# Kernel tuning notes

Measured on AMD Instinct MI355X. Metric: run time of the kernel, lower is better.

The kernel has to match this reference:

```python
import jax, jax.numpy as jnp
import numpy as np

N, C, T, V = 16, 64, 512, 25
R, O, S = 8, 64, 3  # rel_channels, out_channels, num_subset


def setup_inputs() -> dict:
    key = jax.random.key(0)
    ks = jax.random.split(key, 12)
    sc = 0.05
    return {
        "x": jax.random.normal(ks[0], (N, C, T, V), jnp.float32),
        "A": jax.random.normal(ks[1], (S, V, V), jnp.float32) * 0.1,
        "alpha": jax.random.normal(ks[2], (1,), jnp.float32) * 0.1,
        "w1": jax.random.normal(ks[3], (S, R, C), jnp.float32) * sc,
        "b1": jax.random.normal(ks[4], (S, R), jnp.float32) * sc,
        "w2": jax.random.normal(ks[5], (S, R, C), jnp.float32) * sc,
        "b2": jax.random.normal(ks[6], (S, R), jnp.float32) * sc,
        "w3": jax.random.normal(ks[7], (S, O, C), jnp.float32) * sc,
        "b3": jax.random.normal(ks[8], (S, O), jnp.float32) * sc,
        "w4": jax.random.normal(ks[9], (S, O, R), jnp.float32) * sc,
        "b4": jax.random.normal(ks[10], (S, O), jnp.float32) * sc,
        "sparse": 0,
    }


def _mask(w, thr):
    # SparseConv2d: magnitude-threshold the 1x1 conv weights at runtime.
    return jnp.where(jnp.abs(w) > thr, w, jnp.zeros_like(w))


def reference(x, A, alpha, w1, b1, w2, b2, w3, b3, w4, b4, sparse):
    thr = jnp.float32(sparse)

    def conv1x1(w, b, inp):  # w [o,c], b [o], inp [n,c,t,v] -> [n,o,t,v]
        return jnp.einsum('oc,nctv->notv', _mask(w, thr), inp) + b[None, :, None, None]

    y = None
    for i in range(A.shape[0]):
        x1 = conv1x1(w1[i], b1[i], x).mean(-2)          # [n,r,v]
        x2 = conv1x1(w2[i], b2[i], x).mean(-2)          # [n,r,v]
        x3 = conv1x1(w3[i], b3[i], x)                   # [n,o,t,v]
        att = jnp.tanh(x1[..., :, None] - x2[..., None, :])  # [n,r,v,v]
        a = jnp.einsum('or,nruv->nouv', _mask(w4[i], thr), att) + b4[i][None, :, None, None]
        a = a * alpha + A[i][None, None]                # [n,o,v,v]
        z = jnp.einsum('ncuv,nctu->nctv', a, x3)        # node aggregation
        y = z if y is None else y + z
    # in_channels == out_channels -> residual is identity
    return jax.nn.relu(y + x)
```

## Files before the change

kernel.cpp:

```cpp
#include <hip/hip_runtime.h>
#include <cmath>

typedef __bf16 bf16x8 __attribute__((ext_vector_type(8)));
typedef float f32x4 __attribute__((ext_vector_type(4)));

namespace {
constexpr int kN = 16, kC = 64, kT = 512, kV = 25, kS = 3, kR = 8, kO = 64;
constexpr int kTV = kT * kV;
constexpr int kTT = 16;
constexpr size_t WS_AFRAG = 102400;
constexpr size_t WS_W3F = WS_AFRAG + (size_t)48 * 131072;
}

__device__ __forceinline__ int swzA(int col, int cbyte) {
  return ((col << 7) + cbyte) ^ ((col & 7) << 4);
}
__device__ __forceinline__ int swzB(int c, int t, int ubyte) {
  return 65536 + (c << 10) + (((t << 6) + ubyte) ^ ((t & 7) << 4));
}

__global__ __launch_bounds__(512) void k1_mean(const float* __restrict__ x,
                                               float* __restrict__ xm) {
  const int bid = blockIdx.x;
  __shared__ float tile[kTV];
  __shared__ float part[25][20];
  const int tid = threadIdx.x;
  const float4* xg4 = (const float4*)(x + (size_t)bid * kTV);
  for (int i4 = tid; i4 < 3200; i4 += 512) ((float4*)tile)[i4] = xg4[i4];
  __syncthreads();
  if (tid < 500) {
    const int v = tid / 20, k = tid % 20;
    float psum = 0.f;
    for (int t = k; t < kT; t += 20) psum += tile[t * 25 + v];
    part[v][k] = psum;
  }
  __syncthreads();
  if (tid < 25) {
    float s = 0.f;
#pragma unroll
    for (int kk = 0; kk < 20; ++kk) s += part[tid][kk];
    xm[bid * 25 + tid] = s * (1.f / 512.f);
  }
}

__global__ __launch_bounds__(256) void k2_attn(
    const float* __restrict__ xm, const float* __restrict__ Ag,
    const float* __restrict__ alpha, const float* __restrict__ w1,
    const float* __restrict__ b1, const float* __restrict__ w2,
    const float* __restrict__ b2, const float* __restrict__ w3,
    const float* __restrict__ w4, const float* __restrict__ b4,
    const int* __restrict__ sparse, unsigned char* __restrict__ ws) {
  const float thr = (float)sparse[0];
  const int b = blockIdx.x;
  const int s = b >> 6, n = (b >> 2) & 15, q = b & 3;
  __shared__ float xm_l[1600];
  __shared__ float x1_l[200], x2_l[200];
  __shared__ float att_l[8 * 625];
  __shared__ float attsum_l[200];
  __shared__ float ag_l[625];
  __shared__ float acs_l[25];
  __shared__ float w4_l[512];
  const int tid = threadIdx.x;
  for (int i = tid; i < 1600; i += 256) xm_l[i] = xm[n * 1600 + i];
  for (int i = tid; i < 512; i += 256) {
    float w = w4[s * 512 + i];
    w4_l[i] = (fabsf(w) > thr) ? w : 0.f;
  }
  for (int i = tid; i < 625; i += 256) ag_l[i] = Ag[s * 625 + i];
  __syncthreads();
  for (int i = tid; i < 400; i += 256) {
    int which = i / 200, idx = i % 200, r = idx / 25, u = idx % 25;
    const float* wrow = (which == 0 ? w1 : w2) + (s * 8 + r) * 64;
    float acc = 0.f;
    for (int cc = 0; cc < 64; ++cc) {
      float w = wrow[cc];
      w = (fabsf(w) > thr) ? w : 0.f;
      acc += w * xm_l[cc * 25 + u];
    }
    acc += (which == 0 ? b1 : b2)[s * 8 + r];
    if (which == 0) x1_l[idx] = acc;
    else x2_l[idx] = acc;
  }
  __syncthreads();
  for (int i = tid; i < 8 * 625; i += 256) {
    int r = i / 625, uv = i % 625, u = uv / 25, v = uv % 25;
    att_l[i] = tanhf(x1_l[r * 25 + u] - x2_l[r * 25 + v]);
  }
  __syncthreads();
  if (tid < 200) {
    int r = tid / 25, v = tid % 25;
    float sum = 0.f;
    for (int u = 0; u < 25; ++u) sum += att_l[r * 625 + u * 25 + v];
    attsum_l[tid] = sum;
  } else if (tid < 225) {
    int v = tid - 200;
    float sum = 0.f;
    for (int u = 0; u < 25; ++u) sum += ag_l[u * 25 + v];
    acs_l[v] = sum;
  }
  __syncthreads();
  const float al = alpha[0];
  unsigned char* afrag = ws + WS_AFRAG + (size_t)(s * 16 + n) * 131072;
  for (int slot = q * 2048 + tid; slot < (q + 1) * 2048; slot += 256) {
    int c = slot >> 7, vt = (slot >> 6) & 1, l = slot & 63;
    int v = vt * 16 + (l & 15), g = l >> 4;
    bf16x8 out;
    if (v < 25) {
      float b4v = b4[s * 64 + c];
#pragma unroll
      for (int j = 0; j < 8; ++j) {
        int u = g * 8 + j;
        float val = 0.f;
        if (u < 25) {
          float acc = 0.f;
#pragma unroll
          for (int r = 0; r < 8; ++r) acc += w4_l[c * 8 + r] * att_l[r * 625 + u * 25 + v];
          val = al * (acc + b4v) + ag_l[u * 25 + v];
        } else if (u == 25) {
          float acc = 0.f;
#pragma unroll
          for (int r = 0; r < 8; ++r) acc += w4_l[c * 8 + r] * attsum_l[r * 25 + v];
          val = al * acc + 25.f * al * b4v + acs_l[v];
        }
        out[j] = (__bf16)val;
      }
    } else {
#pragma unroll
      for (int j = 0; j < 8; ++j) out[j] = (__bf16)0.f;
    }
    *(bf16x8*)(afrag + (size_t)slot * 16) = out;
  }
  if (n == 0 && tid < 128) {
    unsigned char* w3f = ws + WS_W3F + (size_t)s * 8192;
    int slot = q * 128 + tid;
    int ot = slot >> 7, ks = (slot >> 6) & 1, l = slot & 63;
    int o = ot * 16 + (l & 15), g = l >> 4;
    bf16x8 out;
#pragma unroll
    for (int j = 0; j < 8; ++j) {
      int cp = ks * 32 + g * 8 + j;
      float w = w3[(s * 64 + o) * 64 + cp];
      out[j] = (__bf16)((fabsf(w) > thr) ? w : 0.f);
    }
    *(bf16x8*)(w3f + slot * 16) = out;
  }
}

__global__ __launch_bounds__(512, 2) void k3_main(const float* __restrict__ x,
                                                  const float* __restrict__ b3,
                                                  const unsigned char* __restrict__ ws,
                                                  float* __restrict__ y) {
  const int n = blockIdx.x;
  const int tb = blockIdx.y;
  extern __shared__ __align__(16) unsigned char smem[];
  const int tid = threadIdx.x;
  const int w = tid >> 6, l = tid & 63, g = l >> 4, l15 = l & 15;

  const float4* xg4 = (const float4*)(x + (size_t)n * kC * kTV);

  for (int idx = tid; idx < 3072; idx += 512) {
    int c = idx / 48, r = idx % 48, t = r / 3, ub = 52 + (r % 3) * 4;
    *(unsigned int*)(smem + swzB(c, t, ub)) = 0u;
  }
  for (int i4 = tid; i4 < 6400; i4 += 512) {
    int c = i4 / 100, r4 = i4 % 100;
    float4 vv = xg4[c * 3200 + tb * 100 + r4];
    float vals[4] = {vv.x, vv.y, vv.z, vv.w};
    int lin = r4 * 4;
#pragma unroll
    for (int kk = 0; kk < 4; ++kk) {
      int t = (lin + kk) / 25, u = (lin + kk) % 25;
      *(__bf16*)(smem + swzA(t * 32 + u, c * 2)) = (__bf16)vals[kk];
    }
  }
  __syncthreads();

  const unsigned char* afrag = ws + WS_AFRAG;
  const unsigned char* w3f = ws + WS_W3F;

  f32x4 zacc[8][2];
#pragma unroll
  for (int cc = 0; cc < 8; ++cc)
#pragma unroll
    for (int vt = 0; vt < 2; ++vt) {
      f32x4 zz = {0.f, 0.f, 0.f, 0.f};
      zacc[cc][vt] = zz;
    }

  for (int s = 0; s < kS; ++s) {
    bf16x8 A1[4][2];
#pragma unroll
    for (int ot = 0; ot < 4; ++ot)
#pragma unroll
      for (int ks = 0; ks < 2; ++ks)
        A1[ot][ks] = *(const bf16x8*)(w3f + s * 8192 + ((ot * 2 + ks) * 64 + l) * 16);
    if (s) __syncthreads();

    f32x4 acc[4][4];
#pragma unroll
    for (int cti = 0; cti < 4; ++cti) {
      int col = w * 64 + cti * 16 + l15;
      bf16x8 bk0 = *(const bf16x8*)(smem + swzA(col, g * 16));
      bf16x8 bk1 = *(const bf16x8*)(smem + swzA(col, 64 + g * 16));
#pragma unroll
      for (int ot = 0; ot < 4; ++ot) {
        f32x4 d = {0.f, 0.f, 0.f, 0.f};
        d = __builtin_amdgcn_mfma_f32_16x16x32_bf16(A1[ot][0], bk0, d, 0, 0, 0);
        d = __builtin_amdgcn_mfma_f32_16x16x32_bf16(A1[ot][1], bk1, d, 0, 0, 0);
        acc[cti][ot] = d;
      }
    }
#pragma unroll
    for (int cti = 0; cti < 4; ++cti) {
      int col = w * 64 + cti * 16 + l15;
      int t = col >> 5, u = col & 31;
      if (u < 25) {
#pragma unroll
        for (int ot = 0; ot < 4; ++ot)
#pragma unroll
          for (int jj = 0; jj < 4; ++jj) {
            int o = ot * 16 + g * 4 + jj;
            *(__bf16*)(smem + swzB(o, t, u * 2)) = (__bf16)acc[cti][ot][jj];
          }
      }
    }
    for (int slot = tid; slot < 1024; slot += 512) {
      int c = slot >> 4, t = slot & 15;
      *(__bf16*)(smem + swzB(c, t, 50)) = (__bf16)b3[s * 64 + c];
    }
    bf16x8 B2[8][2];
    const unsigned char* af = afrag + (size_t)(s * 16 + n) * 131072;
#pragma unroll
    for (int cc = 0; cc < 8; ++cc) {
      int c = w * 8 + cc;
#pragma unroll
      for (int vt = 0; vt < 2; ++vt)
        B2[cc][vt] = *(const bf16x8*)(af + ((c * 2 + vt) * 64 + l) * 16);
    }
    __syncthreads();
#pragma unroll
    for (int cc = 0; cc < 8; ++cc) {
      int c = w * 8 + cc;
      bf16x8 a2 = *(const bf16x8*)(smem + swzB(c, l15, g * 16));
      zacc[cc][0] = __builtin_amdgcn_mfma_f32_16x16x32_bf16(a2, B2[cc][0], zacc[cc][0], 0, 0, 0);
      zacc[cc][1] = __builtin_amdgcn_mfma_f32_16x16x32_bf16(a2, B2[cc][1], zacc[cc][1], 0, 0, 0);
    }
  }
  __syncthreads();
  float* zs = (float*)smem;
#pragma unroll
  for (int cc = 0; cc < 8; ++cc) {
    int c = w * 8 + cc;
#pragma unroll
    for (int vt = 0; vt < 2; ++vt) {
      int v = vt * 16 + l15;
      if (v < 25) {
#pragma unroll
        for (int jj = 0; jj < 4; ++jj) {
          int t = g * 4 + jj;
          zs[c * 400 + t * 25 + v] = zacc[cc][vt][jj];
        }
      }
    }
  }
  __syncthreads();
  float4* yg4 = (float4*)(y + (size_t)n * kC * kTV);
  for (int i4 = tid; i4 < 6400; i4 += 512) {
    int c = i4 / 100, r4 = i4 % 100;
    float4 xv = xg4[c * 3200 + tb * 100 + r4];
    float4 zv = *(const float4*)(zs + c * 400 + r4 * 4);
    float4 o;
    o.x = fmaxf(zv.x + xv.x, 0.f);
    o.y = fmaxf(zv.y + xv.y, 0.f);
    o.z = fmaxf(zv.z + xv.z, 0.f);
    o.w = fmaxf(zv.w + xv.w, 0.f);
    yg4[c * 3200 + tb * 100 + r4] = o;
  }
}

extern "C" void kernel_launch(void* const* d_in, const int* in_sizes, int n_in,
                              void* d_out, int out_size, void* d_ws, size_t ws_size,
                              hipStream_t stream) {
  const float* x = (const float*)d_in[0];
  const float* Ag = (const float*)d_in[1];
  const float* alpha = (const float*)d_in[2];
  const float* w1 = (const float*)d_in[3];
  const float* b1 = (const float*)d_in[4];
  const float* w2 = (const float*)d_in[5];
  const float* b2 = (const float*)d_in[6];
  const float* w3 = (const float*)d_in[7];
  const float* b3 = (const float*)d_in[8];
  const float* w4 = (const float*)d_in[9];
  const float* b4 = (const float*)d_in[10];
  const int* sparse = (const int*)d_in[11];

  unsigned char* ws = (unsigned char*)d_ws;
  float* xm = (float*)ws;
  float* y = (float*)d_out;

  static bool attr_set = false;
  if (!attr_set) {
    hipFuncSetAttribute((const void*)k3_main,
                        hipFuncAttributeMaxDynamicSharedMemorySize, 131072);
    attr_set = true;
  }

  k1_mean<<<kN * kC, 512, 0, stream>>>(x, xm);
  k2_attn<<<kS * kN * 4, 256, 0, stream>>>(xm, Ag, alpha, w1, b1, w2, b2, w3, w4,
                                           b4, sparse, ws);
  dim3 g3(kN, kT / kTT);
  k3_main<<<g3, 512, 131072, stream>>>(x, b3, ws, y);
}
```

Baseline: 88.27 us.

## Pre-transpose x to swizzled bf16 tiles in workspace and reuse in main kernel

The mean kernel becomes a transpose kernel: each block converts one (n, time-block) slab of x into the swizzled bf16 shared-memory image, writes per-block partial sums, and stores the image to workspace. A small reduction kernel then finishes the means. The main kernel copies this prebuilt tile straight into LDS and reads the residual from the same bf16 tile instead of reading fp32 x twice. This removes the repeated fp32 reads of x and the in-kernel transposition, at the cost of an extra workspace write and read, an extra launch, and a residual added in bf16 precision. It also changes the swzB XOR swizzle to reduce LDS bank conflicts, splits the epilogue into two halves, and drops the occupancy hint on launch bounds.

New measurement: 94.11 us. +6.6%, slower.

```diff
diff --git a/kernel.cpp b/kernel.cpp
--- a/kernel.cpp
+++ b/kernel.cpp
@@ -5,41 +5,73 @@
 typedef float f32x4 __attribute__((ext_vector_type(4)));
 
 namespace {
-constexpr int kN = 16, kC = 64, kT = 512, kV = 25, kS = 3, kR = 8, kO = 64;
+constexpr int kN = 16, kC = 64, kT = 512, kV = 25, kS = 3, kO = 64;
 constexpr int kTV = kT * kV;
-constexpr int kTT = 16;
 constexpr size_t WS_AFRAG = 102400;
 constexpr size_t WS_W3F = WS_AFRAG + (size_t)48 * 131072;
+constexpr size_t WS_XTR = WS_W3F + 3 * 8192;
+constexpr size_t WS_PSUM = WS_XTR + (size_t)512 * 65536;
 }
 
 __device__ __forceinline__ int swzA(int col, int cbyte) {
   return ((col << 7) + cbyte) ^ ((col & 7) << 4);
 }
 __device__ __forceinline__ int swzB(int c, int t, int ubyte) {
-  return 65536 + (c << 10) + (((t << 6) + ubyte) ^ ((t & 7) << 4));
-}
-
-__global__ __launch_bounds__(512) void k1_mean(const float* __restrict__ x,
-                                               float* __restrict__ xm) {
-  const int bid = blockIdx.x;
-  __shared__ float tile[kTV];
-  __shared__ float part[25][20];
+  return 65536 + (c << 10) +
+         (((t << 6) + ubyte) ^ ((((t & 7) ^ ((c >> 2) & 7)) << 4)));
+}
+
+__global__ __launch_bounds__(256) void k1_tr(const float* __restrict__ x,
+                                             unsigned char* __restrict__ ws) {
+  const int n = blockIdx.x, tb = blockIdx.y;
+  __shared__ __align__(16) unsigned char tile[65536];
   const int tid = threadIdx.x;
-  const float4* xg4 = (const float4*)(x + (size_t)bid * kTV);
-  for (int i4 = tid; i4 < 3200; i4 += 512) ((float4*)tile)[i4] = xg4[i4];
-  __syncthreads();
-  if (tid < 500) {
-    const int v = tid / 20, k = tid % 20;
-    float psum = 0.f;
-    for (int t = k; t < kT; t += 20) psum += tile[t * 25 + v];
-    part[v][k] = psum;
-  }
-  __syncthreads();
-  if (tid < 25) {
+  const float4* xg4 = (const float4*)(x + (size_t)n * kC * kTV);
+  for (int i4 = tid; i4 < 6400; i4 += 256) {
+    int c = i4 / 100, r4 = i4 % 100;
+    float4 vv = xg4[c * 3200 + tb * 100 + r4];
+    float vals[4] = {vv.x, vv.y, vv.z, vv.w};
+    int lin = r4 * 4;
+#pragma unroll
+    for (int k = 0; k < 4; ++k) {
+      int t = (lin + k) / 25, u = (lin + k) % 25;
+      *(__bf16*)(tile + swzA(t * 32 + u, c * 2)) = (__bf16)vals[k];
+    }
+  }
+  for (int idx = tid; idx < 896; idx += 256) {
+    int col_i = idx >> 3, gb = idx & 7;
+    int t = col_i / 7, u = 25 + col_i % 7;
+    f32x4 z = {0.f, 0.f, 0.f, 0.f};
+    *(f32x4*)(tile + swzA(t * 32 + u, gb * 16)) = z;
+  }
+  __syncthreads();
+  float* psum = (float*)(ws + WS_PSUM);
+  for (int i = tid; i < 1600; i += 256) {
+    int c = i / 25, v = i % 25;
     float s = 0.f;
 #pragma unroll
-    for (int kk = 0; kk < 20; ++kk) s += part[tid][kk];
-    xm[bid * 25 + tid] = s * (1.f / 512.f);
+    for (int t = 0; t < 16; ++t)
+      s += (float)(*(const __bf16*)(tile + swzA(t * 32 + v, c * 2)));
+    psum[((size_t)n * 1600 + i) * 32 + tb] = s;
+  }
+  f32x4* dst = (f32x4*)(ws + WS_XTR + (size_t)(n * 32 + tb) * 65536);
+  const f32x4* srcl = (const f32x4*)tile;
+  for (int idx = tid; idx < 4096; idx += 256) dst[idx] = srcl[idx];
+}
+
+__global__ __launch_bounds__(256) void k1_red(const unsigned char* __restrict__ ws_c,
+                                              float* __restrict__ xm) {
+  const float* psum = (const float*)(ws_c + WS_PSUM);
+  const int n = blockIdx.x, tid = threadIdx.x;
+  for (int i = tid; i < 1600; i += 256) {
+    const float4* p = (const float4*)(psum + ((size_t)n * 1600 + i) * 32);
+    float s = 0.f;
+#pragma unroll
+    for (int q = 0; q < 8; ++q) {
+      float4 v = p[q];
+      s += v.x + v.y + v.z + v.w;
+    }
+    xm[n * 1600 + i] = s * (1.f / 512.f);
   }
 }
 
@@ -146,32 +178,23 @@
   }
 }
 
-__global__ __launch_bounds__(512, 2) void k3_main(const float* __restrict__ x,
-                                                  const float* __restrict__ b3,
-                                                  const unsigned char* __restrict__ ws,
-                                                  float* __restrict__ y) {
+__global__ __launch_bounds__(512) void k3_main(const float* __restrict__ b3,
+                                               const unsigned char* __restrict__ ws,
+                                               float* __restrict__ y) {
   const int n = blockIdx.x;
   const int tb = blockIdx.y;
   extern __shared__ __align__(16) unsigned char smem[];
   const int tid = threadIdx.x;
   const int w = tid >> 6, l = tid & 63, g = l >> 4, l15 = l & 15;
 
-  const float4* xg4 = (const float4*)(x + (size_t)n * kC * kTV);
-
   for (int idx = tid; idx < 3072; idx += 512) {
     int c = idx / 48, r = idx % 48, t = r / 3, ub = 52 + (r % 3) * 4;
     *(unsigned int*)(smem + swzB(c, t, ub)) = 0u;
   }
-  for (int i4 = tid; i4 < 6400; i4 += 512) {
-    int c = i4 / 100, r4 = i4 % 100;
-    float4 vv = xg4[c * 3200 + tb * 100 + r4];
-    float vals[4] = {vv.x, vv.y, vv.z, vv.w};
-    int lin = r4 * 4;
-#pragma unroll
-    for (int kk = 0; kk < 4; ++kk) {
-      int t = (lin + kk) / 25, u = (lin + kk) % 25;
-      *(__bf16*)(smem + swzA(t * 32 + u, c * 2)) = (__bf16)vals[kk];
-    }
+  {
+    const f32x4* src = (const f32x4*)(ws + WS_XTR + (size_t)(n * 32 + tb) * 65536);
+    f32x4* dstl = (f32x4*)smem;
+    for (int idx = tid; idx < 4096; idx += 512) dstl[idx] = src[idx];
   }
   __syncthreads();
 
@@ -247,34 +270,40 @@
     }
   }
   __syncthreads();
-  float* zs = (float*)smem;
-#pragma unroll
-  for (int cc = 0; cc < 8; ++cc) {
-    int c = w * 8 + cc;
-#pragma unroll
-    for (int vt = 0; vt < 2; ++vt) {
-      int v = vt * 16 + l15;
-      if (v < 25) {
-#pragma unroll
-        for (int jj = 0; jj < 4; ++jj) {
-          int t = g * 4 + jj;
-          zs[c * 400 + t * 25 + v] = zacc[cc][vt][jj];
+  float* zs = (float*)(smem + 65536);
+  float4* yg4 = (float4*)(y + (size_t)n * kC * kTV);
+#pragma unroll
+  for (int h = 0; h < 2; ++h) {
+    if ((w >> 2) == h) {
+      int c0 = (w & 3) * 8;
+#pragma unroll
+      for (int cc = 0; cc < 8; ++cc)
+#pragma unroll
+        for (int vt = 0; vt < 2; ++vt) {
+          int v = vt * 16 + l15;
+          if (v < 25) {
+#pragma unroll
+            for (int jj = 0; jj < 4; ++jj)
+              zs[(c0 + cc) * 400 + (g * 4 + jj) * 25 + v] = zacc[cc][vt][jj];
+          }
         }
+    }
+    __syncthreads();
+    for (int i4 = tid; i4 < 3200; i4 += 512) {
+      int cl = i4 / 100, r4 = i4 % 100, c = h * 32 + cl;
+      f32x4 zv = *(const f32x4*)(zs + cl * 400 + r4 * 4);
+      float o[4];
+#pragma unroll
+      for (int k = 0; k < 4; ++k) {
+        int lin = r4 * 4 + k, t = lin / 25, u = lin % 25;
+        float xv = (float)(*(const __bf16*)(smem + swzA(t * 32 + u, c * 2)));
+        o[k] = fmaxf(zv[k] + xv, 0.f);
       }
-    }
-  }
-  __syncthreads();
-  float4* yg4 = (float4*)(y + (size_t)n * kC * kTV);
-  for (int i4 = tid; i4 < 6400; i4 += 512) {
-    int c = i4 / 100, r4 = i4 % 100;
-    float4 xv = xg4[c * 3200 + tb * 100 + r4];
-    float4 zv = *(const float4*)(zs + c * 400 + r4 * 4);
-    float4 o;
-    o.x = fmaxf(zv.x + xv.x, 0.f);
-    o.y = fmaxf(zv.y + xv.y, 0.f);
-    o.z = fmaxf(zv.z + xv.z, 0.f);
-    o.w = fmaxf(zv.w + xv.w, 0.f);
-    yg4[c * 3200 + tb * 100 + r4] = o;
+      float4 ov;
+      ov.x = o[0]; ov.y = o[1]; ov.z = o[2]; ov.w = o[3];
+      yg4[c * 3200 + tb * 100 + r4] = ov;
+    }
+    __syncthreads();
   }
 }
 
@@ -298,16 +327,14 @@
   float* xm = (float*)ws;
   float* y = (float*)d_out;
 
-  static bool attr_set = false;
-  if (!attr_set) {
-    hipFuncSetAttribute((const void*)k3_main,
-                        hipFuncAttributeMaxDynamicSharedMemorySize, 131072);
-    attr_set = true;
-  }
-
-  k1_mean<<<kN * kC, 512, 0, stream>>>(x, xm);
+  hipFuncSetAttribute((const void*)k3_main,
+                      hipFuncAttributeMaxDynamicSharedMemorySize, 131072);
+
+  dim3 g1(kN, 32);
+  k1_tr<<<g1, 256, 0, stream>>>(x, ws);
+  k1_red<<<kN, 256, 0, stream>>>(ws, xm);
   k2_attn<<<kS * kN * 4, 256, 0, stream>>>(xm, Ag, alpha, w1, b1, w2, b2, w3, w4,
                                            b4, sparse, ws);
-  dim3 g3(kN, kT / kTT);
-  k3_main<<<g3, 512, 131072, stream>>>(x, b3, ws, y);
-}
+  dim3 g3(kN, kT / 16);
+  k3_main<<<g3, 512, 131072, stream>>>(b3, ws, y);
+}
```
